# Kernel tuning notes

Hardware: AMD Instinct MI355X
Metric: run time of the kernel (lower is better)

The kernel has to match this reference:

```python
import jax, jax.numpy as jnp
import numpy as np

EMBED_DIM = 1024
NUM_HEADS = 16


def setup_inputs() -> dict:
    key = jax.random.key(0)
    kq, kk, kv = jax.random.split(key, 3)
    N, L, S, E = 4, 2048, 2048, EMBED_DIM
    return {
        "query": jax.random.normal(kq, (N, L, E), dtype=jnp.float32),
        "key": jax.random.normal(kk, (N, S, E), dtype=jnp.float32),
        "value": jax.random.normal(kv, (N, S, E), dtype=jnp.float32),
        "is_causal": 1,
    }


def reference(query, key, value, is_causal):
    N, L, E = query.shape
    _, S, E_v = value.shape
    H = NUM_HEADS
    dh = E // H
    dh_v = E_v // H
    # (N, H, L, dh) layout
    q = query.reshape(N, L, H, dh).transpose(0, 2, 1, 3)
    k = key.reshape(N, S, H, dh).transpose(0, 2, 1, 3)
    v = value.reshape(N, S, H, dh_v).transpose(0, 2, 1, 3)

    scale = 1.0 / np.sqrt(dh).astype(np.float32)
    # full LxS score matrix, as in the original (non-flash)
    scores = jnp.einsum('nhld,nhsd->nhls', q, k) * scale
    if is_causal:
        causal = jnp.tril(jnp.ones((L, S), dtype=bool))  # True = allowed
        scores = jnp.where(causal, scores, jnp.float32(-jnp.inf))
    attn_weight = jax.nn.softmax(scores, axis=-1)  # (N,H,L,S)
    y = jnp.einsum('nhls,nhsd->nhld', attn_weight, v)
    y = y.transpose(0, 2, 1, 3).reshape(N, L, E_v)
    return (y, attn_weight)
```

## Files before the change

### kernel.cpp

```cpp
#include <hip/hip_runtime.h>
#include <math.h>
#include <stdint.h>

#define N_B 4
#define N_H 16
#define L_Q 2048
#define L_K 2048
#define E_D 1024
#define DH  64
#define QB  128
#define KB  64
#define NT  512
#define NQT (L_Q / QB)
#define NKT (L_K / KB)
#define LDP  72
#define LDPV 68

typedef _Float16 f16x2 __attribute__((ext_vector_type(2)));
typedef _Float16 f16x4 __attribute__((ext_vector_type(4)));
typedef _Float16 f16x8 __attribute__((ext_vector_type(8)));
typedef float    f32x4 __attribute__((ext_vector_type(4)));

__device__ __forceinline__ f16x4 pk4(float a, float b, float c, float d) {
    f16x2 lo = __builtin_bit_cast(f16x2, __builtin_amdgcn_cvt_pkrtz(a, b));
    f16x2 hi = __builtin_bit_cast(f16x2, __builtin_amdgcn_cvt_pkrtz(c, d));
    f16x4 r; r[0] = lo[0]; r[1] = lo[1]; r[2] = hi[0]; r[3] = hi[1];
    return r;
}

__device__ __forceinline__ void gload16(const _Float16* g, _Float16* l) {
    __builtin_amdgcn_global_load_lds(
        (const __attribute__((address_space(1))) void*)g,
        (__attribute__((address_space(3))) void*)l, 16, 0, 0);
}

__global__ __launch_bounds__(256)
void cvt_qk(const float* __restrict__ Q, const float* __restrict__ K,
            _Float16* __restrict__ Qh, _Float16* __restrict__ Kh)
{
    size_t i = ((size_t)blockIdx.x * 256 + threadIdx.x) * 8;
    float4 a = *(const float4*)(Q + i);
    float4 b = *(const float4*)(Q + i + 4);
    *(f16x4*)(Qh + i)     = pk4(a.x, a.y, a.z, a.w);
    *(f16x4*)(Qh + i + 4) = pk4(b.x, b.y, b.z, b.w);
    float4 c = *(const float4*)(K + i);
    float4 d = *(const float4*)(K + i + 4);
    *(f16x4*)(Kh + i)     = pk4(c.x, c.y, c.z, c.w);
    *(f16x4*)(Kh + i + 4) = pk4(d.x, d.y, d.z, d.w);
}

__global__ __launch_bounds__(256)
void cvt_vt(const float* __restrict__ V, _Float16* __restrict__ Vt)
{
    __shared__ _Float16 T[64][72];
    const int bid = blockIdx.x;
    const int st  = bid & 31;
    const int nh  = bid >> 5;
    const int n   = nh >> 4;
    const int h   = nh & 15;
    const int t   = threadIdx.x;
    const float* Vb = V + ((size_t)(n * L_K + st * 64)) * E_D + h * DH;
    #pragma unroll
    for (int i = 0; i < 4; ++i) {
        int lin = t + i * 256;
        int s = lin >> 4, d = (lin & 15) * 4;
        float4 v = *(const float4*)(Vb + (size_t)s * E_D + d);
        T[d + 0][s] = (_Float16)v.x; T[d + 1][s] = (_Float16)v.y;
        T[d + 2][s] = (_Float16)v.z; T[d + 3][s] = (_Float16)v.w;
    }
    __syncthreads();
    _Float16* Ob = Vt + ((size_t)nh * DH) * L_K + st * 64;
    #pragma unroll
    for (int j = 0; j < 2; ++j) {
        int lin = t + j * 256;
        int d = lin >> 3, sc = (lin & 7) * 8;
        *(f16x8*)(Ob + (size_t)d * L_K + sc) = *(const f16x8*)&T[d][sc];
    }
}

__global__ __launch_bounds__(NT)
void mha_main(const _Float16* __restrict__ Qh, const _Float16* __restrict__ Kh,
              const _Float16* __restrict__ Vth, const int* __restrict__ causp,
              float* __restrict__ Yg, float* __restrict__ Wg)
{
    __shared__ __attribute__((aligned(16))) _Float16 KsL[2][KB * DH];
    __shared__ __attribute__((aligned(16))) _Float16 VsL[2][DH * KB];
    __shared__ __attribute__((aligned(16))) _Float16 Ps[QB][LDP];
    __shared__ float linv[QB];

    const int tid  = threadIdx.x;
    const int lane = tid & 63;
    const int wid  = tid >> 6;
    const int bid0 = blockIdx.x;
    const int bid  = ((bid0 & 7) << 7) + (bid0 >> 3);
    const int qt   = (NQT - 1) - (bid & (NQT - 1));
    const int nh   = bid >> 4;
    const int q0   = qt * QB;
    const int n    = nh >> 4;
    const int h    = nh & 15;
    const bool causal = (*causp) != 0;
    const float scale = 0.125f;

    const int lrow = lane & 15;
    const int g    = lane >> 4;
    const int rb   = wid * 16;
    const int rsub = g * 4;
    const int kt_end = causal ? (2 * qt + 2) : NKT;

    float*  Ybase = Yg + ((size_t)(n * L_Q + q0)) * E_D + h * DH;
    float*  Wbase = Wg + ((size_t)nh * L_Q + q0) * L_K;

    const int srow = wid * 8 + (lane >> 3);
    const int scol = (((lane & 7) ^ ((lane >> 3) & 7)) << 3);
    const _Float16* Ksrc0 = Kh  + ((size_t)(n * L_K) + srow) * E_D + h * DH + scol;
    const _Float16* Vsrc0 = Vth + ((size_t)nh * DH + srow) * L_K + scol;

    const int swz = (lrow & 7) << 4;
    const int cb0 = ((g * 16) ^ swz) >> 1;
    const int cb1 = ((64 + g * 16) ^ swz) >> 1;

    const _Float16* Qrow = Qh + ((size_t)(n * L_Q + q0 + rb + lrow)) * E_D + h * DH;
    const f16x8 qf0 = *(const f16x8*)(Qrow + g * 8);
    const f16x8 qf1 = *(const f16x8*)(Qrow + 32 + g * 8);

    #define STAGE_K(b, kt) gload16(Ksrc0 + (size_t)(kt) * KB * E_D, &KsL[b][wid * 512])
    #define STAGE_KV(b, kt) gload16(Ksrc0 + (size_t)(kt) * KB * E_D, &VsL[b][wid * 512])
    #define STAGE_V(b, kt) gload16(Vsrc0 + (size_t)(kt) * KB,       &VsL[b][wid * 512])
    #define FRAG(buf, tc, half) (*(const f16x8*)&(buf)[(size_t)((tc) * 16 + lrow) * 64 + ((half) ? cb1 : cb0)])

    float l_part = 0.0f;
    {
        const int np = kt_end >> 1;
        STAGE_K(0, 0);
        STAGE_KV(0, 1);
        for (int p = 0; p < np; ++p) {
            __builtin_amdgcn_sched_barrier(0);
            asm volatile("s_waitcnt vmcnt(0) lgkmcnt(0)" ::: "memory");
            __builtin_amdgcn_s_barrier();
            __builtin_amdgcn_sched_barrier(0);
            if (p + 1 < np) {
                STAGE_K((p + 1) & 1, 2 * p + 2);
                STAGE_KV((p + 1) & 1, 2 * p + 3);
            }
            #pragma unroll
            for (int half = 0; half < 2; ++half) {
                const int kt = 2 * p + half;
                const _Float16* Kc = half ? &VsL[p & 1][0] : &KsL[p & 1][0];
                f32x4 acc[4] = {};
                #pragma unroll
                for (int tc = 0; tc < 4; ++tc) {
                    acc[tc] = __builtin_amdgcn_mfma_f32_16x16x32_f16(FRAG(Kc, tc, 0), qf0, acc[tc], 0, 0, 0);
                    acc[tc] = __builtin_amdgcn_mfma_f32_16x16x32_f16(FRAG(Kc, tc, 1), qf1, acc[tc], 0, 0, 0);
                }
                const bool dm = causal && (kt >= 2 * qt);
                const int krel = (kt - 2 * qt) * 64;
                #pragma unroll
                for (int tc = 0; tc < 4; ++tc) {
                    #pragma unroll
                    for (int i = 0; i < 4; ++i) {
                        float v = acc[tc][i] * scale;
                        bool ok = !dm || (krel + tc * 16 + rsub + i <= rb + lrow);
                        l_part += ok ? __expf(v) : 0.0f;
                    }
                }
            }
        }
        __syncthreads();
    }
    l_part += __shfl_xor(l_part, 16);
    l_part += __shfl_xor(l_part, 32);
    const float inv_l = 1.0f / l_part;
    linv[rb + lrow] = inv_l;

    f32x4 o[4] = {};
    STAGE_K(0, 0);
    STAGE_V(0, 0);
    __syncthreads();

    float winv[4];
    #pragma unroll
    for (int j = 0; j < 4; ++j) winv[j] = linv[rb + (lane >> 4) + 4 * j];

    for (int kt = 0; kt < kt_end; ++kt) {
        const int cur = kt & 1;
        if (kt + 1 < kt_end) { STAGE_K(cur ^ 1, kt + 1); STAGE_V(cur ^ 1, kt + 1); }

        f32x4 acc[4] = {};
        #pragma unroll
        for (int tc = 0; tc < 4; ++tc) {
            acc[tc] = __builtin_amdgcn_mfma_f32_16x16x32_f16(FRAG(KsL[cur], tc, 0), qf0, acc[tc], 0, 0, 0);
            acc[tc] = __builtin_amdgcn_mfma_f32_16x16x32_f16(FRAG(KsL[cur], tc, 1), qf1, acc[tc], 0, 0, 0);
        }

        const bool dm = causal && (kt >= 2 * qt);
        const int krel = (kt - 2 * qt) * 64;
        #pragma unroll
        for (int tc = 0; tc < 4; ++tc) {
            float v, p0, p1, p2, p3;
            v = acc[tc][0] * scale;
            p0 = (!dm || (krel + tc * 16 + rsub + 0 <= rb + lrow)) ? __expf(v) : 0.0f;
            v = acc[tc][1] * scale;
            p1 = (!dm || (krel + tc * 16 + rsub + 1 <= rb + lrow)) ? __expf(v) : 0.0f;
            v = acc[tc][2] * scale;
            p2 = (!dm || (krel + tc * 16 + rsub + 2 <= rb + lrow)) ? __expf(v) : 0.0f;
            v = acc[tc][3] * scale;
            p3 = (!dm || (krel + tc * 16 + rsub + 3 <= rb + lrow)) ? __expf(v) : 0.0f;
            *(f16x4*)&Ps[rb + lrow][tc * 16 + rsub] = pk4(p0, p1, p2, p3);
        }

        f16x8 pf0 = *(const f16x8*)&Ps[rb + lrow][0 + g * 8];
        f16x8 pf1 = *(const f16x8*)&Ps[rb + lrow][32 + g * 8];
        #pragma unroll
        for (int tc = 0; tc < 4; ++tc) {
            o[tc] = __builtin_amdgcn_mfma_f32_16x16x32_f16(FRAG(VsL[cur], tc, 0), pf0, o[tc], 0, 0, 0);
            o[tc] = __builtin_amdgcn_mfma_f32_16x16x32_f16(FRAG(VsL[cur], tc, 1), pf1, o[tc], 0, 0, 0);
        }

        {
            float* Wt = Wbase + (size_t)kt * KB;
            const int c0 = (lane & 15) * 4;
            #pragma unroll
            for (int j = 0; j < 4; ++j) {
                const int rl = rb + (lane >> 4) + 4 * j;
                f16x4 pv = *(const f16x4*)&Ps[rl][c0];
                const float s = winv[j];
                f32x4 wv = { (float)pv[0] * s, (float)pv[1] * s,
                             (float)pv[2] * s, (float)pv[3] * s };
                __builtin_nontemporal_store(wv, (f32x4*)(Wt + (size_t)rl * L_K + c0));
            }
        }

        __builtin_amdgcn_sched_barrier(0);
        asm volatile("s_waitcnt vmcnt(4) lgkmcnt(0)" ::: "memory");
        __builtin_amdgcn_s_barrier();
        __builtin_amdgcn_sched_barrier(0);
    }

    #pragma unroll
    for (int tc = 0; tc < 4; ++tc) {
        f32x4 yv = { o[tc][0] * inv_l, o[tc][1] * inv_l,
                     o[tc][2] * inv_l, o[tc][3] * inv_l };
        __builtin_nontemporal_store(yv, (f32x4*)(Ybase + (size_t)(rb + lrow) * E_D + tc * 16 + rsub));
    }

    if (causal && kt_end < NKT) {
        const int c0 = kt_end * KB;
        const int rem4 = (L_K - c0) >> 2;
        const f32x4 z = { 0.f, 0.f, 0.f, 0.f };
        for (int r = 0; r < QB; ++r) {
            float* row = Wbase + (size_t)r * L_K + c0;
            for (int c4 = tid; c4 < rem4; c4 += NT) {
                __builtin_nontemporal_store(z, (f32x4*)(row + c4 * 4));
            }
        }
    }
    #undef STAGE_K
    #undef STAGE_KV
    #undef STAGE_V
    #undef FRAG
}

__global__ __launch_bounds__(256)
void mha_fwd_fallback(const float* __restrict__ Qg, const float* __restrict__ Kg,
                      const float* __restrict__ Vg, const int* __restrict__ causp,
                      float* __restrict__ Yg, float* __restrict__ Wg)
{
    __shared__ __attribute__((aligned(16))) _Float16 Qs[64][LDP];
    __shared__ __attribute__((aligned(16))) _Float16 Ks[64][LDP];
    __shared__ __attribute__((aligned(16))) _Float16 Psf[64][LDP];
    __shared__ __attribute__((aligned(16))) _Float16 Vt[DH][LDPV];

    const int tid  = threadIdx.x;
    const int lane = tid & 63;
    const int wid  = tid >> 6;
    const int bid  = blockIdx.x;
    const int qt   = bid & 31;
    const int nh   = bid >> 5;
    const int q0   = qt * 64;
    const int n    = nh >> 4;
    const int h    = nh & 15;
    const bool causal = (*causp) != 0;
    const float scale = 0.125f;

    const float* Qbase = Qg + ((size_t)(n * L_Q + q0)) * E_D + h * DH;
    const float* Kbase = Kg + ((size_t)n * L_K) * E_D + h * DH;
    const float* Vbase = Vg + ((size_t)n * L_K) * E_D + h * DH;
    float*       Ybase = Yg + ((size_t)(n * L_Q + q0)) * E_D + h * DH;
    float*       Wbase = Wg + ((size_t)nh * L_Q + q0) * L_K;

    const int lrow = lane & 15;
    const int lk   = (lane >> 4) * 8;
    const int rb   = wid * 16;
    const int rsub = (lane >> 4) * 4;
    const int kt_end = causal ? (qt + 1) : NKT;

    #pragma unroll
    for (int i = 0; i < 4; ++i) {
        int lin = tid + i * 256;
        int r = lin >> 4;
        int c = (lin & 15) * 4;
        float4 qv = *(const float4*)(Qbase + (size_t)r * E_D + c);
        *(f16x4*)&Qs[r][c] = pk4(qv.x, qv.y, qv.z, qv.w);
    }
    __syncthreads();
    const f16x8 qf0 = *(const f16x8*)&Qs[rb + lrow][lk];
    const f16x8 qf1 = *(const f16x8*)&Qs[rb + lrow][32 + lk];

    float l_part = 0.0f;
    for (int kt = 0; kt < kt_end; ++kt) {
        const float* Kt = Kbase + (size_t)kt * KB * E_D;
        __syncthreads();
        #pragma unroll
        for (int i = 0; i < 4; ++i) {
            int lin = tid + i * 256;
            int r = lin >> 4;
            int c = (lin & 15) * 4;
            float4 kv = *(const float4*)(Kt + (size_t)r * E_D + c);
            *(f16x4*)&Ks[r][c] = pk4(kv.x, kv.y, kv.z, kv.w);
        }
        __syncthreads();
        f32x4 acc[4] = {};
        #pragma unroll
        for (int tc = 0; tc < 4; ++tc) {
            f16x8 a0 = *(const f16x8*)&Ks[tc * 16 + lrow][lk];
            f16x8 a1 = *(const f16x8*)&Ks[tc * 16 + lrow][32 + lk];
            acc[tc] = __builtin_amdgcn_mfma_f32_16x16x32_f16(a0, qf0, acc[tc], 0, 0, 0);
            acc[tc] = __builtin_amdgcn_mfma_f32_16x16x32_f16(a1, qf1, acc[tc], 0, 0, 0);
        }
        const bool dm = causal && (kt == qt);
        #pragma unroll
        for (int tc = 0; tc < 4; ++tc) {
            #pragma unroll
            for (int i = 0; i < 4; ++i) {
                float v = acc[tc][i] * scale;
                bool ok = !dm || (tc * 16 + rsub + i <= rb + lrow);
                l_part += ok ? __expf(v) : 0.0f;
            }
        }
    }
    l_part += __shfl_xor(l_part, 16);
    l_part += __shfl_xor(l_part, 32);
    const float inv_l = 1.0f / l_part;

    f32x4 o[4] = {};
    for (int kt = 0; kt < kt_end; ++kt) {
        const float* Kt  = Kbase + (size_t)kt * KB * E_D;
        const float* Vtg = Vbase + (size_t)kt * KB * E_D;
        __syncthreads();
        #pragma unroll
        for (int i = 0; i < 4; ++i) {
            int lin = tid + i * 256;
            int r = lin >> 4;
            int c = (lin & 15) * 4;
            float4 kv = *(const float4*)(Kt + (size_t)r * E_D + c);
            *(f16x4*)&Ks[r][c] = pk4(kv.x, kv.y, kv.z, kv.w);
            int d   = lin & 63;
            int kk0 = (lin >> 6) * 4;
            float v0 = Vtg[(size_t)(kk0 + 0) * E_D + d];
            float v1 = Vtg[(size_t)(kk0 + 1) * E_D + d];
            float v2 = Vtg[(size_t)(kk0 + 2) * E_D + d];
            float v3 = Vtg[(size_t)(kk0 + 3) * E_D + d];
            *(f16x4*)&Vt[d][kk0] = pk4(v0, v1, v2, v3);
        }
        __syncthreads();
        f32x4 acc[4] = {};
        #pragma unroll
        for (int tc = 0; tc < 4; ++tc) {
            f16x8 a0 = *(const f16x8*)&Ks[tc * 16 + lrow][lk];
            f16x8 a1 = *(const f16x8*)&Ks[tc * 16 + lrow][32 + lk];
            acc[tc] = __builtin_amdgcn_mfma_f32_16x16x32_f16(a0, qf0, acc[tc], 0, 0, 0);
            acc[tc] = __builtin_amdgcn_mfma_f32_16x16x32_f16(a1, qf1, acc[tc], 0, 0, 0);
        }
        const bool dm = causal && (kt == qt);
        float* Wrow = Wbase + (size_t)(rb + lrow) * L_K + kt * KB;
        #pragma unroll
        for (int tc = 0; tc < 4; ++tc) {
            float v, p0, p1, p2, p3;
            v = acc[tc][0] * scale;
            p0 = (!dm || (tc * 16 + rsub + 0 <= rb + lrow)) ? __expf(v) : 0.0f;
            v = acc[tc][1] * scale;
            p1 = (!dm || (tc * 16 + rsub + 1 <= rb + lrow)) ? __expf(v) : 0.0f;
            v = acc[tc][2] * scale;
            p2 = (!dm || (tc * 16 + rsub + 2 <= rb + lrow)) ? __expf(v) : 0.0f;
            v = acc[tc][3] * scale;
            p3 = (!dm || (tc * 16 + rsub + 3 <= rb + lrow)) ? __expf(v) : 0.0f;
            float4 wv = make_float4(p0 * inv_l, p1 * inv_l, p2 * inv_l, p3 * inv_l);
            *(float4*)(Wrow + tc * 16 + rsub) = wv;
            *(f16x4*)&Psf[rb + lrow][tc * 16 + rsub] = pk4(p0, p1, p2, p3);
        }
        f16x8 pf0 = *(const f16x8*)&Psf[rb + lrow][lk];
        f16x8 pf1 = *(const f16x8*)&Psf[rb + lrow][32 + lk];
        #pragma unroll
        for (int tc = 0; tc < 4; ++tc) {
            f16x4 t0 = *(const f16x4*)&Vt[tc * 16 + lrow][lk];
            f16x4 t1 = *(const f16x4*)&Vt[tc * 16 + lrow][lk + 4];
            f16x8 a0 = __builtin_shufflevector(t0, t1, 0, 1, 2, 3, 4, 5, 6, 7);
            f16x4 t2 = *(const f16x4*)&Vt[tc * 16 + lrow][32 + lk];
            f16x4 t3 = *(const f16x4*)&Vt[tc * 16 + lrow][32 + lk + 4];
            f16x8 a1 = __builtin_shufflevector(t2, t3, 0, 1, 2, 3, 4, 5, 6, 7);
            o[tc] = __builtin_amdgcn_mfma_f32_16x16x32_f16(a0, pf0, o[tc], 0, 0, 0);
            o[tc] = __builtin_amdgcn_mfma_f32_16x16x32_f16(a1, pf1, o[tc], 0, 0, 0);
        }
    }
    #pragma unroll
    for (int tc = 0; tc < 4; ++tc) {
        float4 yv = make_float4(o[tc][0] * inv_l, o[tc][1] * inv_l,
                                o[tc][2] * inv_l, o[tc][3] * inv_l);
        *(float4*)(Ybase + (size_t)(rb + lrow) * E_D + tc * 16 + rsub) = yv;
    }
    if (causal && kt_end < NKT) {
        const int c0 = kt_end * KB;
        const int rem4 = (L_K - c0) >> 2;
        const float4 z = make_float4(0.f, 0.f, 0.f, 0.f);
        for (int r = 0; r < 64; ++r) {
            float* row = Wbase + (size_t)r * L_K + c0;
            for (int c4 = tid; c4 < rem4; c4 += 256) {
                *(float4*)(row + c4 * 4) = z;
            }
        }
    }
}

extern "C" void kernel_launch(void* const* d_in, const int* in_sizes, int n_in,
                              void* d_out, int out_size, void* d_ws, size_t ws_size,
                              hipStream_t stream) {
    const float* Q  = (const float*)d_in[0];
    const float* K  = (const float*)d_in[1];
    const float* V  = (const float*)d_in[2];
    const int* caus = (const int*)d_in[3];
    float* Y = (float*)d_out;
    float* W = (float*)d_out + (size_t)N_B * L_Q * E_D;

    const size_t elems = (size_t)N_B * L_Q * E_D;
    const size_t need  = 3 * elems * sizeof(_Float16);

    if (ws_size >= need) {
        _Float16* Qh = (_Float16*)d_ws;
        _Float16* Kh = Qh + elems;
        _Float16* Vt = Kh + elems;
        hipLaunchKernelGGL(cvt_qk, dim3(elems / (256 * 8)), dim3(256), 0, stream, Q, K, Qh, Kh);
        hipLaunchKernelGGL(cvt_vt, dim3(N_B * N_H * (L_K / 64)), dim3(256), 0, stream, V, Vt);
        hipLaunchKernelGGL(mha_main, dim3(N_B * N_H * NQT), dim3(NT), 0, stream,
                           Qh, Kh, Vt, caus, Y, W);
    } else {
        hipLaunchKernelGGL(mha_fwd_fallback, dim3(N_B * N_H * 32), dim3(256), 0, stream,
                           Q, K, V, caus, Y, W);
    }
}
```

Baseline: 276.1 us.

## Convert Q in-kernel and read K directly from global in row-sum pass

Removes the separate fp16 conversion of Q by loading fp32 Q rows inside the attention kernel and packing them to fp16 in registers, which shrinks the workspace and the pre-pass traffic. The first pass, which computes softmax denominators, now loads K fragments straight from global memory instead of staging double-buffered tiles through LDS with barriers. This removes synchronisation and LDS traffic in that pass. The cost is uncoalesced, latency-exposed global loads that rely on cache hits.

```diff
diff --git a/kernel.cpp b/kernel.cpp
--- a/kernel.cpp
+++ b/kernel.cpp
@@ -28,6 +28,12 @@
     return r;
 }
 
+__device__ __forceinline__ f16x8 pk8(float4 a, float4 b) {
+    f16x4 lo = pk4(a.x, a.y, a.z, a.w);
+    f16x4 hi = pk4(b.x, b.y, b.z, b.w);
+    return __builtin_shufflevector(lo, hi, 0, 1, 2, 3, 4, 5, 6, 7);
+}
+
 __device__ __forceinline__ void gload16(const _Float16* g, _Float16* l) {
     __builtin_amdgcn_global_load_lds(
         (const __attribute__((address_space(1))) void*)g,
@@ -35,14 +41,9 @@
 }
 
 __global__ __launch_bounds__(256)
-void cvt_qk(const float* __restrict__ Q, const float* __restrict__ K,
-            _Float16* __restrict__ Qh, _Float16* __restrict__ Kh)
+void cvt_k(const float* __restrict__ K, _Float16* __restrict__ Kh)
 {
     size_t i = ((size_t)blockIdx.x * 256 + threadIdx.x) * 8;
-    float4 a = *(const float4*)(Q + i);
-    float4 b = *(const float4*)(Q + i + 4);
-    *(f16x4*)(Qh + i)     = pk4(a.x, a.y, a.z, a.w);
-    *(f16x4*)(Qh + i + 4) = pk4(b.x, b.y, b.z, b.w);
     float4 c = *(const float4*)(K + i);
     float4 d = *(const float4*)(K + i + 4);
     *(f16x4*)(Kh + i)     = pk4(c.x, c.y, c.z, c.w);
@@ -79,7 +80,7 @@
 }
 
 __global__ __launch_bounds__(NT)
-void mha_main(const _Float16* __restrict__ Qh, const _Float16* __restrict__ Kh,
+void mha_main(const float* __restrict__ Qg, const _Float16* __restrict__ Kh,
               const _Float16* __restrict__ Vth, const int* __restrict__ causp,
               float* __restrict__ Yg, float* __restrict__ Wg)
 {
@@ -119,53 +120,41 @@
     const int cb0 = ((g * 16) ^ swz) >> 1;
     const int cb1 = ((64 + g * 16) ^ swz) >> 1;
 
-    const _Float16* Qrow = Qh + ((size_t)(n * L_Q + q0 + rb + lrow)) * E_D + h * DH;
-    const f16x8 qf0 = *(const f16x8*)(Qrow + g * 8);
-    const f16x8 qf1 = *(const f16x8*)(Qrow + 32 + g * 8);
+    const float* Qrowf = Qg + ((size_t)(n * L_Q + q0 + rb + lrow)) * E_D + h * DH;
+    const f16x8 qf0 = pk8(*(const float4*)(Qrowf + g * 8),
+                          *(const float4*)(Qrowf + g * 8 + 4));
+    const f16x8 qf1 = pk8(*(const float4*)(Qrowf + 32 + g * 8),
+                          *(const float4*)(Qrowf + 32 + g * 8 + 4));
 
     #define STAGE_K(b, kt) gload16(Ksrc0 + (size_t)(kt) * KB * E_D, &KsL[b][wid * 512])
-    #define STAGE_KV(b, kt) gload16(Ksrc0 + (size_t)(kt) * KB * E_D, &VsL[b][wid * 512])
     #define STAGE_V(b, kt) gload16(Vsrc0 + (size_t)(kt) * KB,       &VsL[b][wid * 512])
     #define FRAG(buf, tc, half) (*(const f16x8*)&(buf)[(size_t)((tc) * 16 + lrow) * 64 + ((half) ? cb1 : cb0)])
 
     float l_part = 0.0f;
     {
-        const int np = kt_end >> 1;
-        STAGE_K(0, 0);
-        STAGE_KV(0, 1);
-        for (int p = 0; p < np; ++p) {
-            __builtin_amdgcn_sched_barrier(0);
-            asm volatile("s_waitcnt vmcnt(0) lgkmcnt(0)" ::: "memory");
-            __builtin_amdgcn_s_barrier();
-            __builtin_amdgcn_sched_barrier(0);
-            if (p + 1 < np) {
-                STAGE_K((p + 1) & 1, 2 * p + 2);
-                STAGE_KV((p + 1) & 1, 2 * p + 3);
-            }
+        const _Float16* Kfr = Kh + ((size_t)(n * L_K) + lrow) * E_D + h * DH + g * 8;
+        for (int kt = 0; kt < kt_end; ++kt) {
+            const _Float16* Kt = Kfr + (size_t)kt * KB * E_D;
+            f32x4 acc[4] = {};
             #pragma unroll
-            for (int half = 0; half < 2; ++half) {
-                const int kt = 2 * p + half;
-                const _Float16* Kc = half ? &VsL[p & 1][0] : &KsL[p & 1][0];
-                f32x4 acc[4] = {};
+            for (int tc = 0; tc < 4; ++tc) {
+                f16x8 a0 = *(const f16x8*)(Kt + (size_t)(tc * 16) * E_D);
+                f16x8 a1 = *(const f16x8*)(Kt + (size_t)(tc * 16) * E_D + 32);
+                acc[tc] = __builtin_amdgcn_mfma_f32_16x16x32_f16(a0, qf0, acc[tc], 0, 0, 0);
+                acc[tc] = __builtin_amdgcn_mfma_f32_16x16x32_f16(a1, qf1, acc[tc], 0, 0, 0);
+            }
+            const bool dm = causal && (kt >= 2 * qt);
+            const int krel = (kt - 2 * qt) * 64;
+            #pragma unroll
+            for (int tc = 0; tc < 4; ++tc) {
                 #pragma unroll
-                for (int tc = 0; tc < 4; ++tc) {
-                    acc[tc] = __builtin_amdgcn_mfma_f32_16x16x32_f16(FRAG(Kc, tc, 0), qf0, acc[tc], 0, 0, 0);
-                    acc[tc] = __builtin_amdgcn_mfma_f32_16x16x32_f16(FRAG(Kc, tc, 1), qf1, acc[tc], 0, 0, 0);
+                for (int i = 0; i < 4; ++i) {
+                    float v = acc[tc][i] * scale;
+                    bool ok = !dm || (krel + tc * 16 + rsub + i <= rb + lrow);
+                    l_part += ok ? __expf(v) : 0.0f;
                 }
-                const bool dm = causal && (kt >= 2 * qt);
-                const int krel = (kt - 2 * qt) * 64;
-                #pragma unroll
-                for (int tc = 0; tc < 4; ++tc) {
-                    #pragma unroll
-                    for (int i = 0; i < 4; ++i) {
-                        float v = acc[tc][i] * scale;
-                        bool ok = !dm || (krel + tc * 16 + rsub + i <= rb + lrow);
-                        l_part += ok ? __expf(v) : 0.0f;
-                    }
-                }
-            }
-        }
-        __syncthreads();
+            }
+        }
     }
     l_part += __shfl_xor(l_part, 16);
     l_part += __shfl_xor(l_part, 32);
@@ -255,7 +244,6 @@
         }
     }
     #undef STAGE_K
-    #undef STAGE_KV
     #undef STAGE_V
     #undef FRAG
 }
@@ -432,16 +420,15 @@
     float* W = (float*)d_out + (size_t)N_B * L_Q * E_D;
 
     const size_t elems = (size_t)N_B * L_Q * E_D;
-    const size_t need  = 3 * elems * sizeof(_Float16);
+    const size_t need  = 2 * elems * sizeof(_Float16);
 
     if (ws_size >= need) {
-        _Float16* Qh = (_Float16*)d_ws;
-        _Float16* Kh = Qh + elems;
+        _Float16* Kh = (_Float16*)d_ws;
         _Float16* Vt = Kh + elems;
-        hipLaunchKernelGGL(cvt_qk, dim3(elems / (256 * 8)), dim3(256), 0, stream, Q, K, Qh, Kh);
+        hipLaunchKernelGGL(cvt_k, dim3(elems / (256 * 8)), dim3(256), 0, stream, K, Kh);
         hipLaunchKernelGGL(cvt_vt, dim3(N_B * N_H * (L_K / 64)), dim3(256), 0, stream, V, Vt);
         hipLaunchKernelGGL(mha_main, dim3(N_B * N_H * NQT), dim3(NT), 0, stream,
-                           Qh, Kh, Vt, caus, Y, W);
+                           Q, Kh, Vt, caus, Y, W);
     } else {
         hipLaunchKernelGGL(mha_fwd_fallback, dim3(N_B * N_H * 32), dim3(256), 0, stream,
                            Q, K, V, caus, Y, W);
```

Measured after the change: 304.2 us. 1.1x slower.
